# Optimization experiments

Hardware: AMD Instinct MI355X
Metric: run time of the kernel (lower is better)

## Reference

```python
import jax, jax.numpy as jnp
import numpy as np

HEAD = 4  # from init_kwargs


def setup_inputs() -> dict:
    key = jax.random.key(0)
    ks = jax.random.split(key, 8)
    B, C, H, W = 32, 512, 64, 64
    s = 1.0 / np.sqrt(C)
    return {
        "x": jax.random.normal(ks[0], (B, C, H, W), dtype=jnp.float32),
        "Wq": jax.random.normal(ks[1], (C, C), dtype=jnp.float32) * s,
        "bq": jax.random.normal(ks[2], (C,), dtype=jnp.float32) * 0.01,
        "Wk": jax.random.normal(ks[3], (C, C), dtype=jnp.float32) * s,
        "bk": jax.random.normal(ks[4], (C,), dtype=jnp.float32) * 0.01,
        "Wv": jax.random.normal(ks[5], (C, C), dtype=jnp.float32) * s,
        "bv": jax.random.normal(ks[6], (C,), dtype=jnp.float32) * 0.01,
        "gamma": jax.random.normal(ks[7], (1,), dtype=jnp.float32),
    }


def reference(x, Wq, bq, Wk, bk, Wv, bv, gamma):
    B, C, H, W = x.shape
    HW = H * W
    d = HW // HEAD  # per-head feature (spatial) dim

    def proj(Wm, bm):
        # 1x1 conv == channel GEMM; then split HW into (head, d) and move head out
        y = jnp.einsum('bchw,oc->bohw', x, Wm) + bm[None, :, None, None]
        return y.reshape(B, C, HEAD, d).transpose(0, 2, 1, 3)  # (B, head, C, d)

    q = proj(Wq, bq)
    k = proj(Wk, bk)
    v = proj(Wv, bv)

    energy = jnp.einsum('bhcd,bhed->bhce', q, k)          # (B, head, C, C)
    attn = jax.nn.softmax(energy, axis=-1)
    out = jnp.einsum('bhce,bhed->bhcd', attn, v)          # (B, head, C, d)
    out = out.transpose(0, 2, 1, 3).reshape(B, C, H, W)
    return gamma[0] * out + x
```

## Files before the change

### kernel.cpp

```cpp
#include <hip/hip_runtime.h>

typedef _Float16 f16;
typedef f16 f16x4 __attribute__((ext_vector_type(4)));
typedef f16 f16x8 __attribute__((ext_vector_type(8)));
typedef float f32x4 __attribute__((ext_vector_type(4)));

#define BATCH 32
#define CCH   512
#define HWSZ  4096
#define PERB  (CCH*HWSZ)
#define EPB   (CCH*CCH)

__global__ __launch_bounds__(256) void wconv_k(
    const float* __restrict__ Wq, const float* __restrict__ Wk,
    const float* __restrict__ Wv, f16* __restrict__ Wqk, f16* __restrict__ Wvh)
{
  const int idx = (blockIdx.x*256 + threadIdx.x)*4;
  float4 q = *(const float4*)(Wq+idx);
  float4 k = *(const float4*)(Wk+idx);
  float4 v = *(const float4*)(Wv+idx);
  f16x4 oq = {(f16)q.x,(f16)q.y,(f16)q.z,(f16)q.w};
  f16x4 ok = {(f16)k.x,(f16)k.y,(f16)k.z,(f16)k.w};
  f16x4 ov = {(f16)v.x,(f16)v.y,(f16)v.z,(f16)v.w};
  *(f16x4*)(Wqk+idx)      = oq;
  *(f16x4*)(Wqk+EPB+idx)  = ok;
  *(f16x4*)(Wvh+idx)      = ov;
}

__global__ __launch_bounds__(256) void transpose_k(
    const float* __restrict__ x, f16* __restrict__ Xt)
{
  __shared__ f16 tile[64][80];
  const int s0 = blockIdx.x*64, c0 = blockIdx.y*64, b = blockIdx.z;
  const int t = threadIdx.x;
  const int r = t>>2, cs = (t&3)*16;
  const float* src = x + (size_t)b*PERB + (size_t)(c0+r)*HWSZ + s0 + cs;
  float4 v0 = *(const float4*)src;
  float4 v1 = *(const float4*)(src+4);
  float4 v2 = *(const float4*)(src+8);
  float4 v3 = *(const float4*)(src+12);
  f16x8 p0 = {(f16)v0.x,(f16)v0.y,(f16)v0.z,(f16)v0.w,(f16)v1.x,(f16)v1.y,(f16)v1.z,(f16)v1.w};
  f16x8 p1 = {(f16)v2.x,(f16)v2.y,(f16)v2.z,(f16)v2.w,(f16)v3.x,(f16)v3.y,(f16)v3.z,(f16)v3.w};
  *(f16x8*)&tile[r][cs]   = p0;
  *(f16x8*)&tile[r][cs+8] = p1;
  __syncthreads();
  f16x8 o0, o1;
  #pragma unroll
  for (int k=0;k<8;k++){ o0[k]=tile[cs+k][r]; o1[k]=tile[cs+8+k][r]; }
  f16* dst = Xt + (size_t)b*PERB + (size_t)(s0+r)*CCH + c0 + cs;
  *(f16x8*)dst     = o0;
  *(f16x8*)(dst+8) = o1;
}

__global__ __launch_bounds__(256) void softmax_k(
    const float* __restrict__ E, f16* __restrict__ P)
{
  const int wv = threadIdx.x>>6, lane = threadIdx.x&63;
  const size_t row = (size_t)blockIdx.x*4 + wv;
  const float* e = E + row*CCH + lane*8;
  float4 a = *(const float4*)e;
  float4 b = *(const float4*)(e+4);
  float v[8] = {a.x,a.y,a.z,a.w,b.x,b.y,b.z,b.w};
  float m = v[0];
  #pragma unroll
  for (int k=1;k<8;k++) m = fmaxf(m, v[k]);
  #pragma unroll
  for (int off=32; off; off>>=1) m = fmaxf(m, __shfl_xor(m, off));
  float s = 0.f;
  #pragma unroll
  for (int k=0;k<8;k++){ v[k] = __expf(v[k]-m); s += v[k]; }
  #pragma unroll
  for (int off=32; off; off>>=1) s += __shfl_xor(s, off);
  const float inv = 1.0f / s;
  f16x8 o;
  #pragma unroll
  for (int k=0;k<8;k++) o[k] = (f16)(v[k]*inv);
  *(f16x8*)(P + row*CCH + lane*8) = o;
}

template<int MODE>
__global__ __launch_bounds__(256) void gemm_k(
    const f16* __restrict__ Aroot, const f16* __restrict__ Broot,
    void* __restrict__ out0, void* __restrict__ out1,
    const float* __restrict__ bias0, const float* __restrict__ bias1,
    const float* __restrict__ xin, const float* __restrict__ gam)
{
  constexpr int K   = (MODE==2) ? 1024 : 512;
  constexpr int LDA = (MODE==2) ? 4096 : 512;
  constexpr int LDB = (MODE==2) ? 4096 : 512;
  constexpr int NT  = K/32;

  const int t  = threadIdx.x;
  const int z  = blockIdx.z;
  const int m0 = blockIdx.y*128, n0 = blockIdx.x*128;

  const f16* Ap; const f16* Bp;
  if constexpr (MODE==0)      { Ap = Aroot;                    Bp = Broot + (size_t)z*PERB; }
  else if constexpr (MODE==1) { Ap = Aroot + (size_t)z*PERB;   Bp = Broot; }
  else if constexpr (MODE==2) { const int b=z>>2, h=z&3;
                                Ap = Aroot + (size_t)b*PERB + h*1024;
                                Bp = Broot + (size_t)b*PERB + h*1024; }
  else                        { const int b=z>>2, h=z&3;
                                Ap = Aroot + (size_t)z*EPB;
                                Bp = Broot + (size_t)b*PERB + (size_t)h*1024*512; }

  __shared__ f16 sA[128*32];
  __shared__ f16 sB[128*32];

  const int sr = t>>2, sc = (t&3)*8;

  f16x8 ra0, ra1, rb0, rb1;
  auto LOADT = [&](int KS) {
    const size_t ko = (size_t)KS + sc;
    ra0 = *(const f16x8*)(Ap + (size_t)(m0+sr)   *LDA + ko);
    ra1 = *(const f16x8*)(Ap + (size_t)(m0+64+sr)*LDA + ko);
    rb0 = *(const f16x8*)(Bp + (size_t)(n0+sr)   *LDB + ko);
    rb1 = *(const f16x8*)(Bp + (size_t)(n0+64+sr)*LDB + ko);
  };

  LOADT(0);

  const f32x4 zero = {0.f,0.f,0.f,0.f};
  f32x4 acc[4][4];
  #pragma unroll
  for (int i=0;i<4;i++)
    #pragma unroll
    for (int j=0;j<4;j++) acc[i][j] = zero;

  const int wv = t>>6, lane = t&63;
  const int wm = (wv>>1)*64, wn = (wv&1)*64;
  const int lrow = lane&15, lk = (lane>>4)*8;

  for (int ks=0; ks<NT; ++ks) {
    __syncthreads();
    *(f16x8*)&sA[ sr    *32 + sc] = ra0;
    *(f16x8*)&sA[(64+sr)*32 + sc] = ra1;
    *(f16x8*)&sB[ sr    *32 + sc] = rb0;
    *(f16x8*)&sB[(64+sr)*32 + sc] = rb1;
    __syncthreads();
    if (ks+1 < NT) LOADT((ks+1)*32);
    f16x8 af[4], bf[4];
    #pragma unroll
    for (int i=0;i<4;i++) af[i] = *(const f16x8*)&sA[(wm + i*16 + lrow)*32 + lk];
    #pragma unroll
    for (int j=0;j<4;j++) bf[j] = *(const f16x8*)&sB[(wn + j*16 + lrow)*32 + lk];
    #pragma unroll
    for (int i=0;i<4;i++)
      #pragma unroll
      for (int j=0;j<4;j++)
        acc[i][j] = __builtin_amdgcn_mfma_f32_16x16x32_f16(af[i], bf[j], acc[i][j], 0,0,0);
  }

  const int rbase = m0 + wm + (lane>>4)*4;
  #pragma unroll
  for (int i=0;i<4;i++) {
    const int row = rbase + i*16;
    #pragma unroll
    for (int j=0;j<4;j++) {
      const int col = n0 + wn + j*16 + lrow;
      f32x4 v = acc[i][j];
      #pragma unroll
      for (int r=0;r<4;r++) {
        const int rr = row + r;
        if constexpr (MODE==0) {
          if (rr < 512)
            ((f16*)out0)[(size_t)z*PERB + (size_t)rr*HWSZ + col]        = (f16)(v[r] + bias0[rr]);
          else
            ((f16*)out1)[(size_t)z*PERB + (size_t)(rr-512)*HWSZ + col]  = (f16)(v[r] + bias1[rr-512]);
        } else if constexpr (MODE==1) {
          ((f16*)out0)[(size_t)z*PERB + (size_t)rr*CCH + col] = (f16)(v[r] + bias0[col]);
        } else if constexpr (MODE==2) {
          ((float*)out0)[(size_t)z*EPB + (size_t)rr*CCH + col] = v[r];
        } else {
          const int b = z>>2, h = z&3;
          const size_t idx = (size_t)b*PERB + (size_t)rr*HWSZ + h*1024 + col;
          ((float*)out0)[idx] = gam[0]*v[r] + xin[idx];
        }
      }
    }
  }
}

extern "C" void kernel_launch(void* const* d_in, const int* in_sizes, int n_in,
                              void* d_out, int out_size, void* d_ws, size_t ws_size,
                              hipStream_t stream)
{
  const float* x  = (const float*)d_in[0];
  const float* Wq = (const float*)d_in[1];
  const float* bq = (const float*)d_in[2];
  const float* Wk = (const float*)d_in[3];
  const float* bk = (const float*)d_in[4];
  const float* Wv = (const float*)d_in[5];
  const float* bv = (const float*)d_in[6];
  const float* gm = (const float*)d_in[7];

  char* ws  = (char*)d_ws;
  f16* Qb   = (f16*)ws;
  f16* Kb   = (f16*)(ws + 134217728ull);
  f16* Wqk  = (f16*)(ws + 268435456ull);
  f16* Wvh  = Wqk + 1024*512;
  f16* Pb   = Qb;
  f16* Vt   = Kb;
  float* E  = (float*)d_out;
  f16*  Xt  = (f16*)((char*)d_out + 134217728ull);
  float* out = (float*)d_out;

  wconv_k    <<<256, 256, 0, stream>>>(Wq, Wk, Wv, Wqk, Wvh);
  transpose_k<<<dim3(64,8,32),  256, 0, stream>>>(x, Xt);
  gemm_k<0>  <<<dim3(32,8,32),  256, 0, stream>>>(Wqk, Xt, Qb, Kb, bq, bk, nullptr, nullptr);
  gemm_k<2>  <<<dim3(4,4,128),  256, 0, stream>>>(Qb, Kb, E, nullptr, nullptr, nullptr, nullptr, nullptr);
  gemm_k<1>  <<<dim3(4,32,32),  256, 0, stream>>>(Xt, Wvh, Vt, nullptr, bv, nullptr, nullptr, nullptr);
  softmax_k  <<<16384, 256, 0, stream>>>(E, Pb);
  gemm_k<3>  <<<dim3(8,4,128),  256, 0, stream>>>(Pb, Vt, out, nullptr, nullptr, nullptr, x, gm);
}
```

Before: 1.406 ms.

## Load GEMM tiles directly into LDS and remap workgroups across XCDs

Replaces the register-staged global→LDS copy and its software prefetch with `__builtin_amdgcn_global_load_lds` direct-to-LDS 16-byte loads, issued per wave for 16-row slices. It also remaps the flat workgroup index so consecutive tiles land on the same XCD, aiming for better L2 reuse. Together these cut VGPR pressure and LDS-store instructions. In exchange, loads are no longer overlapped with the previous tile's MFMA work, since the loop is now load, barrier, compute with a single buffer. That may expose global-memory latency.

```diff
diff --git a/kernel.cpp b/kernel.cpp
--- a/kernel.cpp
+++ b/kernel.cpp
@@ -10,6 +10,12 @@
 #define HWSZ  4096
 #define PERB  (CCH*HWSZ)
 #define EPB   (CCH*CCH)
+
+typedef __attribute__((address_space(3))) uint32_t lds_u32;
+typedef const __attribute__((address_space(1))) uint32_t glb_u32;
+__device__ __forceinline__ void gload16(const void* g, void* l) {
+  __builtin_amdgcn_global_load_lds((glb_u32*)(uintptr_t)g, (lds_u32*)(uintptr_t)l, 16, 0, 0);
+}
 
 __global__ __launch_bounds__(256) void wconv_k(
     const float* __restrict__ Wq, const float* __restrict__ Wk,
@@ -89,10 +95,18 @@
   constexpr int LDA = (MODE==2) ? 4096 : 512;
   constexpr int LDB = (MODE==2) ? 4096 : 512;
   constexpr int NT  = K/32;
+  constexpr int GX  = (MODE==0)?32 : (MODE==1)?4 : (MODE==2)?4 : 8;
+  constexpr int GY  = (MODE==0)?8  : (MODE==1)?32: 4;
+  constexpr int GZ  = (MODE==0||MODE==1)?32 : 128;
+  constexpr int NWG = GX*GY*GZ;
+
+  int flat = blockIdx.x + GX*(blockIdx.y + GY*blockIdx.z);
+  flat = (flat & 7)*(NWG/8) + (flat >> 3);
+  const int bx = flat % GX;  const int rem = flat / GX;
+  const int by = rem % GY;   const int z  = rem / GY;
 
   const int t  = threadIdx.x;
-  const int z  = blockIdx.z;
-  const int m0 = blockIdx.y*128, n0 = blockIdx.x*128;
+  const int m0 = by*128, n0 = bx*128;
 
   const f16* Ap; const f16* Bp;
   if constexpr (MODE==0)      { Ap = Aroot;                    Bp = Broot + (size_t)z*PERB; }
@@ -107,18 +121,16 @@
   __shared__ f16 sA[128*32];
   __shared__ f16 sB[128*32];
 
-  const int sr = t>>2, sc = (t&3)*8;
-
-  f16x8 ra0, ra1, rb0, rb1;
-  auto LOADT = [&](int KS) {
-    const size_t ko = (size_t)KS + sc;
-    ra0 = *(const f16x8*)(Ap + (size_t)(m0+sr)   *LDA + ko);
-    ra1 = *(const f16x8*)(Ap + (size_t)(m0+64+sr)*LDA + ko);
-    rb0 = *(const f16x8*)(Bp + (size_t)(n0+sr)   *LDB + ko);
-    rb1 = *(const f16x8*)(Bp + (size_t)(n0+64+sr)*LDB + ko);
-  };
-
-  LOADT(0);
+  const int wv = t>>6, lane = t&63;
+  const int srow = lane>>2, scol = (lane&3)*8;
+  f16* sA0 = sA + (wv*32)*32;
+  f16* sA1 = sA + (wv*32+16)*32;
+  f16* sB0 = sB + (wv*32)*32;
+  f16* sB1 = sB + (wv*32+16)*32;
+  const f16* gA0 = Ap + (size_t)(m0 + wv*32 + srow)*LDA + scol;
+  const f16* gA1 = gA0 + (size_t)16*LDA;
+  const f16* gB0 = Bp + (size_t)(n0 + wv*32 + srow)*LDB + scol;
+  const f16* gB1 = gB0 + (size_t)16*LDB;
 
   const f32x4 zero = {0.f,0.f,0.f,0.f};
   f32x4 acc[4][4];
@@ -127,18 +139,17 @@
     #pragma unroll
     for (int j=0;j<4;j++) acc[i][j] = zero;
 
-  const int wv = t>>6, lane = t&63;
   const int wm = (wv>>1)*64, wn = (wv&1)*64;
   const int lrow = lane&15, lk = (lane>>4)*8;
 
   for (int ks=0; ks<NT; ++ks) {
+    if (ks) __syncthreads();
+    const int ko = ks*32;
+    gload16(gA0 + ko, sA0);
+    gload16(gA1 + ko, sA1);
+    gload16(gB0 + ko, sB0);
+    gload16(gB1 + ko, sB1);
     __syncthreads();
-    *(f16x8*)&sA[ sr    *32 + sc] = ra0;
-    *(f16x8*)&sA[(64+sr)*32 + sc] = ra1;
-    *(f16x8*)&sB[ sr    *32 + sc] = rb0;
-    *(f16x8*)&sB[(64+sr)*32 + sc] = rb1;
-    __syncthreads();
-    if (ks+1 < NT) LOADT((ks+1)*32);
     f16x8 af[4], bf[4];
     #pragma unroll
     for (int i=0;i<4;i++) af[i] = *(const f16x8*)&sA[(wm + i*16 + lrow)*32 + lk];
```

Result: faster. 1.262 ms (-10.3%).
